# Kernel optimization log

Measured on AMD Instinct MI355X. Metric: run time of the kernel, lower is better.

Reference implementation:

```python
import jax, jax.numpy as jnp
import numpy as np

B, S, E = 4, 2048, 768
DFF = 4 * E
EPS = 1e-5


def _layernorm(x, g, b):
    mu = jnp.mean(x, axis=-1, keepdims=True)
    var = jnp.mean(jnp.square(x - mu), axis=-1, keepdims=True)
    return (x - mu) * jax.lax.rsqrt(var + EPS) * g + b


def setup_inputs() -> dict:
    key = jax.random.key(0)
    ks = jax.random.split(key, 16)
    w = lambda k, shp: jax.random.normal(k, shp, dtype=jnp.float32) * 0.02
    inp = {
        "x": jax.random.normal(ks[0], (B, S, E), dtype=jnp.float32),
        "kv": jax.random.normal(ks[1], (B, S, E), dtype=jnp.float32),
        "wq_w": w(ks[2], (E, E)), "wq_b": jnp.zeros((E,), jnp.float32),
        "wk_w": w(ks[3], (E, E)), "wk_b": jnp.zeros((E,), jnp.float32),
        "wv_w": w(ks[4], (E, E)), "wv_b": jnp.zeros((E,), jnp.float32),
        "ln1_g": jnp.ones((E,), jnp.float32), "ln1_b": jnp.zeros((E,), jnp.float32),
        "wq2_w": w(ks[5], (E, E)), "wq2_b": jnp.zeros((E,), jnp.float32),
        "wk2_w": w(ks[6], (E, E)), "wk2_b": jnp.zeros((E,), jnp.float32),
        "wv2_w": w(ks[7], (E, E)), "wv2_b": jnp.zeros((E,), jnp.float32),
        "ln2_g": jnp.ones((E,), jnp.float32), "ln2_b": jnp.zeros((E,), jnp.float32),
        "w1": w(ks[8], (DFF, E)), "b1": jnp.zeros((DFF,), jnp.float32),
        "w2": w(ks[9], (E, DFF)), "b2": jnp.zeros((E,), jnp.float32),
        "ln3_g": jnp.ones((E,), jnp.float32), "ln3_b": jnp.zeros((E,), jnp.float32),
    }
    return inp


def reference(x, kv, wq_w, wq_b, wk_w, wk_b, wv_w, wv_b, ln1_g, ln1_b,
              wq2_w, wq2_b, wk2_w, wk2_b, wv2_w, wv2_b, ln2_g, ln2_b,
              w1, b1, w2, b2, ln3_g, ln3_b):
    scalar = 1.0 / np.sqrt(E).astype(np.float32)
    mask_value = jnp.finfo(x.dtype).min
    s = x.shape[1]
    causal = jnp.triu(jnp.ones((s, s), dtype=bool), k=1)  # True above diagonal -> masked

    # ---- causal self-attention (single head, full E) ----
    q = x @ wq_w.T + wq_b
    k = x @ wk_w.T + wk_b
    v = x @ wv_w.T + wv_b
    scores = jnp.einsum('bqe,bke->bqk', q, k) * scalar
    scores = jnp.where(causal, mask_value, scores)
    h1 = jnp.einsum('bqk,bke->bqe', jax.nn.softmax(scores, axis=-1), v)
    x = _layernorm(x + h1, ln1_g, ln1_b)

    # ---- cross-attention over kv (no mask) ----
    q2 = x @ wq2_w.T + wq2_b
    k2 = kv @ wk2_w.T + wk2_b
    v2 = kv @ wv2_w.T + wv2_b
    scores2 = jnp.einsum('bqe,bke->bqk', q2, k2) * scalar
    h2 = jnp.einsum('bqk,bke->bqe', jax.nn.softmax(scores2, axis=-1), v2)
    x = _layernorm(x + h2, ln2_g, ln2_b)

    # ---- MLP: Linear -> ReLU -> Linear -> ReLU (note trailing ReLU) ----
    h = jax.nn.relu(x @ w1.T + b1)
    mlp = jax.nn.relu(h @ w2.T + b2)
    return _layernorm(x + mlp, ln3_g, ln3_b)
```

## Files before the change

### kernel.cpp

```cpp
#include <hip/hip_runtime.h>
#include <hip/hip_bf16.h>
#include <math.h>


typedef __bf16 bf16_t;
typedef bf16_t bf16x8 __attribute__((ext_vector_type(8)));
typedef float f32x4 __attribute__((ext_vector_type(4)));

#define TBM 128
#define TBN 128
#define TBK 32
#define CPAD 136

struct MMDesc {
    const bf16_t* A;
    const bf16_t* B;
    const float* bias;
    __hip_bfloat16* C;
    float* lsum;
    int koff;
    int trans;
};
struct MMArgs { MMDesc g[8]; };

__device__ __forceinline__ void load16(const bf16_t* g, bf16_t* l) {
    __builtin_amdgcn_global_load_lds(
        (const __attribute__((address_space(1))) unsigned int*)g,
        (__attribute__((address_space(3))) unsigned int*)l, 16, 0, 0);
}

__device__ __forceinline__ void mm_core(
    const bf16_t* Ag, const bf16_t* Bg, int lda, int ldb, int K,
    bf16_t* Asm, bf16_t* Bsm, int w, int l, int wm, int wn, f32x4 acc[4][4]) {
    const int fr = l & 15;
    const int kq = (l >> 4) * 8;
    const long rsA = (long)64 * lda, rsB = (long)64 * ldb;
    bf16_t* Al = Asm + w * 512;
    bf16_t* Bl = Bsm + w * 512;

    for (int k0 = 0; k0 < K; k0 += 64) {
        load16(Ag + k0, Al);
        load16(Ag + rsA + k0, Al + 2048);
        load16(Bg + k0, Bl);
        load16(Bg + rsB + k0, Bl + 2048);
        load16(Ag + k0 + 32, Al + 4096);
        load16(Ag + rsA + k0 + 32, Al + 6144);
        load16(Bg + k0 + 32, Bl + 4096);
        load16(Bg + rsB + k0 + 32, Bl + 6144);
        __syncthreads();

#pragma unroll
        for (int t = 0; t < 2; ++t) {
            const bf16_t* As = Asm + t * 4096;
            const bf16_t* Bs = Bsm + t * 4096;
            bf16x8 af[4], bfr[4];
#pragma unroll
            for (int i = 0; i < 4; ++i)
                af[i] = *(const bf16x8*)(As + (wm + i * 16 + fr) * TBK + kq);
#pragma unroll
            for (int j = 0; j < 4; ++j)
                bfr[j] = *(const bf16x8*)(Bs + (wn + j * 16 + fr) * TBK + kq);
#pragma unroll
            for (int i = 0; i < 4; ++i)
#pragma unroll
                for (int j = 0; j < 4; ++j)
                    acc[i][j] = __builtin_amdgcn_mfma_f32_16x16x32_bf16(
                        af[i], bfr[j], acc[i][j], 0, 0, 0);
        }
        __syncthreads();
    }
}

__device__ __forceinline__ void tile_out(
    const __hip_bfloat16* ct, __hip_bfloat16* base, long ldc, int tid) {
#pragma unroll
    for (int u = 0; u < 8; ++u) {
        const int e = u * 2048 + tid * 8;
        const int rl = e >> 7, cl = e & 127;
        *(uint4*)(base + (long)rl * ldc + cl) = *(const uint4*)(ct + rl * CPAD + cl);
    }
}

template <bool RELU, bool CLAMPK>
__global__ __launch_bounds__(256) void mm_std(
    MMArgs args, int M, int N, int K, int lda, int ldb, float scale, int GX) {
    __shared__ __align__(16) bf16_t smem[128 * CPAD];
    bf16_t* Asm = smem;
    bf16_t* Bsm = smem + 8192;

    const MMDesc dsc = args.g[blockIdx.z];

    const int lin = blockIdx.x;
    const int panel = lin / (8 * GX);
    const int rem = lin - panel * 8 * GX;
    const int bx = rem >> 3;
    const int by = panel * 8 + (rem & 7);

    const int m0 = by * TBM, n0 = bx * TBN;
    const int tid = threadIdx.x, w = tid >> 6, l = tid & 63;
    const int wm = (w >> 1) * 64, wn = (w & 1) * 64;
    const int srow = w * 16 + (l >> 2);
    const int scol = (l & 3) * 8;
    const int fr = l & 15;

    f32x4 acc[4][4];
    const f32x4 z4 = {0.f, 0.f, 0.f, 0.f};
#pragma unroll
    for (int i = 0; i < 4; ++i)
#pragma unroll
        for (int j = 0; j < 4; ++j) acc[i][j] = z4;

    int Keff = K;
    if (CLAMPK) {
        int km = (by + 1) * TBM - dsc.koff;
        Keff = km < K ? km : K;
    }
    if (!CLAMPK || Keff > 0)
        mm_core(dsc.A + (long)(m0 + srow) * lda + scol,
                dsc.B + (long)(n0 + srow) * ldb + scol,
                lda, ldb, Keff, Asm, Bsm, w, l, wm, wn, acc);

    __hip_bfloat16* ct = (__hip_bfloat16*)smem;
    const int erow = (l >> 4) * 4;
#pragma unroll
    for (int j = 0; j < 4; ++j) {
        const int cl = wn + j * 16 + fr;
        const float bv = dsc.bias ? dsc.bias[n0 + cl] : 0.f;
#pragma unroll
        for (int i = 0; i < 4; ++i) {
            const int rl = wm + i * 16 + erow;
#pragma unroll
            for (int r = 0; r < 4; ++r) {
                float v = acc[i][j][r] * scale + bv;
                if (RELU) v = fmaxf(v, 0.f);
                const int idx = dsc.trans ? (cl * CPAD + rl + r) : ((rl + r) * CPAD + cl);
                ct[idx] = __float2bfloat16(v);
            }
        }
    }
    __syncthreads();
    __hip_bfloat16* base;
    long ldc;
    if (dsc.trans) {
        base = dsc.C + ((long)(m0 >> 11) * N + n0) * 2048 + (m0 & 2047);
        ldc = 2048;
    } else {
        base = dsc.C + (long)m0 * N + n0;
        ldc = N;
    }
    tile_out(ct, base, ldc, tid);
}

template <bool CAUSAL>
__global__ __launch_bounds__(256) void mm_exp(
    MMArgs args, int N, int K, int lda, int ldb, float scale, int GX) {
    __shared__ __align__(16) bf16_t smem[128 * CPAD];
    bf16_t* Asm = smem;
    bf16_t* Bsm = smem + 8192;

    const MMDesc dsc = args.g[blockIdx.z];

    int bx, by;
    if (CAUSAL) {
        const int t = blockIdx.x;
        by = (int)((sqrtf(8.f * t + 1.f) - 1.f) * 0.5f);
        while ((by + 1) * (by + 2) / 2 <= t) ++by;
        while (by * (by + 1) / 2 > t) --by;
        bx = t - by * (by + 1) / 2;
    } else {
        const int lin = blockIdx.x;
        const int panel = lin / (8 * GX);
        const int rem = lin - panel * 8 * GX;
        bx = rem >> 3;
        by = panel * 8 + (rem & 7);
    }

    const int m0 = by * TBM, n0 = bx * TBN;
    const int tid = threadIdx.x, w = tid >> 6, l = tid & 63;
    const int wm = (w >> 1) * 64, wn = (w & 1) * 64;
    const int srow = w * 16 + (l >> 2);
    const int scol = (l & 3) * 8;
    const int fr = l & 15;

    f32x4 acc[4][4];
    const f32x4 z4 = {0.f, 0.f, 0.f, 0.f};
#pragma unroll
    for (int i = 0; i < 4; ++i)
#pragma unroll
        for (int j = 0; j < 4; ++j) acc[i][j] = z4;

    mm_core(dsc.A + (long)(m0 + srow) * lda + scol,
            dsc.B + (long)(n0 + srow) * ldb + scol,
            lda, ldb, K, Asm, Bsm, w, l, wm, wn, acc);

    __hip_bfloat16* ct = (__hip_bfloat16*)smem;
    const int erow = (l >> 4) * 4;
#pragma unroll
    for (int i = 0; i < 4; ++i) {
#pragma unroll
        for (int r = 0; r < 4; ++r) {
            const int rl = wm + i * 16 + erow + r;
            const int grow = m0 + rl;
            float rs = 0.f;
#pragma unroll
            for (int j = 0; j < 4; ++j) {
                const int cl = wn + j * 16 + fr;
                float e;
                if (CAUSAL && (n0 + cl) > grow)
                    e = 0.f;
                else
                    e = __expf(acc[i][j][r] * scale);
                ct[rl * CPAD + cl] = __float2bfloat16(e);
                rs += e;
            }
#pragma unroll
            for (int o = 8; o > 0; o >>= 1) rs += __shfl_down(rs, o, 16);
            if ((l & 15) == 0) atomicAdd(&dsc.lsum[grow], rs);
        }
    }
    __syncthreads();
    tile_out(ct, dsc.C + (long)m0 * N + n0, N, tid);
}

__device__ __forceinline__ float waveReduceSum(float v) {
#pragma unroll
    for (int o = 32; o > 0; o >>= 1) v += __shfl_down(v, o, 64);
    return v;
}
__device__ __forceinline__ float blockReduceSum(float v, float* s) {
    int lane = threadIdx.x & 63, w = threadIdx.x >> 6;
    v = waveReduceSum(v);
    __syncthreads();
    if (lane == 0) s[w] = v;
    __syncthreads();
    return s[0] + s[1] + s[2] + s[3];
}

template <bool BR, bool XF32>
__global__ __launch_bounds__(256) void ln_kernel(
    const float* __restrict__ xf, const __hip_bfloat16* __restrict__ xh,
    const __hip_bfloat16* __restrict__ h1, const __hip_bfloat16* __restrict__ h2,
    const float* __restrict__ hbias, const float* __restrict__ lsum,
    const float* __restrict__ g, const float* __restrict__ beta,
    float* __restrict__ outf, __hip_bfloat16* __restrict__ outb) {
    __shared__ float red[4];
    const int E = 768;
    const long row = blockIdx.x;
    const float hscale = lsum ? (1.f / lsum[row]) : 1.f;

    float vals[3];
    float sum = 0.f;
#pragma unroll
    for (int i = 0; i < 3; ++i) {
        int c = threadIdx.x + i * 256;
        float t = __bfloat162float(h1[row * E + c]) + __bfloat162float(h2[row * E + c]);
        if (BR) t = fmaxf(t + hbias[c], 0.f);
        else t *= hscale;
        float xv = XF32 ? xf[row * E + c] : __bfloat162float(xh[row * E + c]);
        vals[i] = xv + t;
        sum += vals[i];
    }
    sum = blockReduceSum(sum, red);
    const float mean = sum * (1.f / 768.f);

    float ss = 0.f;
#pragma unroll
    for (int i = 0; i < 3; ++i) {
        float d = vals[i] - mean;
        ss += d * d;
    }
    ss = blockReduceSum(ss, red);
    const float inv = rsqrtf(ss * (1.f / 768.f) + 1e-5f);

#pragma unroll
    for (int i = 0; i < 3; ++i) {
        int c = threadIdx.x + i * 256;
        float v = (vals[i] - mean) * inv * g[c] + beta[c];
        if (outf) outf[row * E + c] = v;
        if (outb) outb[row * E + c] = __float2bfloat16(v);
    }
}

struct CvtPtrs {
    const float* s[10];
    __hip_bfloat16* d[10];
};
__global__ __launch_bounds__(256) void cvt_all(CvtPtrs p) {
    int bid = blockIdx.x, seg, off;
    if (bid < 3456) {
        seg = bid / 576;
        off = (bid % 576) * 1024;
    } else if (bid < 8064) {
        int t = bid - 3456;
        seg = 6 + t / 2304;
        off = (t % 2304) * 1024;
    } else {
        int t = bid - 8064;
        seg = 8 + t / 6144;
        off = (t % 6144) * 1024;
    }
    const float* s = p.s[seg];
    __hip_bfloat16* d = p.d[seg];
    int i = off + threadIdx.x * 4;
    float4 v = *(const float4*)(s + i);
    d[i + 0] = __float2bfloat16(v.x);
    d[i + 1] = __float2bfloat16(v.y);
    d[i + 2] = __float2bfloat16(v.z);
    d[i + 3] = __float2bfloat16(v.w);
}

extern "C" void kernel_launch(void* const* d_in, const int* in_sizes, int n_in,
                              void* d_out, int out_size, void* d_ws, size_t ws_size,
                              hipStream_t stream) {
    const int Bb = 4, S = 2048, E = 768, DFF = 3072;
    const int Nr = Bb * S;

    const float* x    = (const float*)d_in[0];
    const float* kv   = (const float*)d_in[1];
    const float* wq_w = (const float*)d_in[2];
    const float* wq_b = (const float*)d_in[3];
    const float* wk_w = (const float*)d_in[4];
    const float* wk_b = (const float*)d_in[5];
    const float* wv_w = (const float*)d_in[6];
    const float* wv_b = (const float*)d_in[7];
    const float* ln1g = (const float*)d_in[8];
    const float* ln1b = (const float*)d_in[9];
    const float* wq2w = (const float*)d_in[10];
    const float* wq2b = (const float*)d_in[11];
    const float* wk2w = (const float*)d_in[12];
    const float* wk2b = (const float*)d_in[13];
    const float* wv2w = (const float*)d_in[14];
    const float* wv2b = (const float*)d_in[15];
    const float* ln2g = (const float*)d_in[16];
    const float* ln2b = (const float*)d_in[17];
    const float* w1   = (const float*)d_in[18];
    const float* b1   = (const float*)d_in[19];
    const float* w2   = (const float*)d_in[20];
    const float* b2   = (const float*)d_in[21];
    const float* ln3g = (const float*)d_in[22];
    const float* ln3b = (const float*)d_in[23];
    float* out = (float*)d_out;

    char* wsp = (char*)d_ws;
    auto alloc = [&](size_t bytes) {
        char* p = wsp;
        wsp += (bytes + 255) & ~(size_t)255;
        return p;
    };
    const size_t nSE = (size_t)Nr * E;
    const size_t nSS = (size_t)Bb * S * S;
    __hip_bfloat16* Pb   = (__hip_bfloat16*)alloc(nSS * 2);
    __hip_bfloat16* qb   = (__hip_bfloat16*)alloc(nSE * 2);
    __hip_bfloat16* kb   = (__hip_bfloat16*)alloc(nSE * 2);
    __hip_bfloat16* hffb = Pb;
    __hip_bfloat16* vtb  = (__hip_bfloat16*)alloc(nSE * 2);
    __hip_bfloat16* xb   = (__hip_bfloat16*)alloc(nSE * 2);
    __hip_bfloat16* kvb  = (__hip_bfloat16*)alloc(nSE * 2);
    __hip_bfloat16* actb = (__hip_bfloat16*)alloc(nSE * 2);
    __hip_bfloat16* hA   = (__hip_bfloat16*)alloc(nSE * 2);
    __hip_bfloat16* hB   = (__hip_bfloat16*)alloc(nSE * 2);
    __hip_bfloat16* wqb   = (__hip_bfloat16*)alloc((size_t)E * E * 2);
    __hip_bfloat16* wkb   = (__hip_bfloat16*)alloc((size_t)E * E * 2);
    __hip_bfloat16* wvb   = (__hip_bfloat16*)alloc((size_t)E * E * 2);
    __hip_bfloat16* wq2bm = (__hip_bfloat16*)alloc((size_t)E * E * 2);
    __hip_bfloat16* wk2bm = (__hip_bfloat16*)alloc((size_t)E * E * 2);
    __hip_bfloat16* wv2bm = (__hip_bfloat16*)alloc((size_t)E * E * 2);
    __hip_bfloat16* w1b   = (__hip_bfloat16*)alloc((size_t)DFF * E * 2);
    __hip_bfloat16* w2b   = (__hip_bfloat16*)alloc((size_t)E * DFF * 2);
    float* lsum1 = (float*)alloc((size_t)Nr * 4);
    float* lsum2 = (float*)alloc((size_t)Nr * 4);

    const float scale = 1.0f / sqrtf((float)E);
    const dim3 blk(256);

    hipMemsetAsync(lsum1, 0, (size_t)Nr * 4 * 2, stream);

    CvtPtrs cp;
    cp.s[0] = wq_w; cp.d[0] = wqb;
    cp.s[1] = wk_w; cp.d[1] = wkb;
    cp.s[2] = wv_w; cp.d[2] = wvb;
    cp.s[3] = wq2w; cp.d[3] = wq2bm;
    cp.s[4] = wk2w; cp.d[4] = wk2bm;
    cp.s[5] = wv2w; cp.d[5] = wv2bm;
    cp.s[6] = w1;   cp.d[6] = w1b;
    cp.s[7] = w2;   cp.d[7] = w2b;
    cp.s[8] = x;    cp.d[8] = xb;
    cp.s[9] = kv;   cp.d[9] = kvb;
    cvt_all<<<8064 + 12288, blk, 0, stream>>>(cp);

    {
        MMArgs a{};
        a.g[0] = {(const bf16_t*)xb, (const bf16_t*)wqb, wq_b, qb, nullptr, 0, 0};
        a.g[1] = {(const bf16_t*)xb, (const bf16_t*)wkb, wk_b, kb, nullptr, 0, 0};
        a.g[2] = {(const bf16_t*)xb, (const bf16_t*)wvb, wv_b, vtb, nullptr, 0, 1};
        mm_std<false, false><<<dim3(6 * 64, 1, 3), blk, 0, stream>>>(
            a, Nr, E, E, E, E, 1.f, 6);
    }
    {
        MMArgs a{};
        for (int b = 0; b < 4; ++b)
            a.g[b] = {(const bf16_t*)qb + (long)b * S * E,
                      (const bf16_t*)kb + (long)b * S * E, nullptr,
                      Pb + (long)b * S * S, lsum1 + b * S, 0, 0};
        mm_exp<true><<<dim3(136, 1, 4), blk, 0, stream>>>(a, S, E, E, E, scale, 16);
    }
    {
        MMArgs a{};
        for (int b = 0; b < 4; ++b)
            for (int ks = 0; ks < 2; ++ks)
                a.g[b * 2 + ks] = {(const bf16_t*)Pb + (long)b * S * S + ks * 1024,
                                   (const bf16_t*)vtb + (long)b * E * S + ks * 1024,
                                   nullptr, (ks ? hB : hA) + (long)b * S * E,
                                   nullptr, ks * 1024, 0};
        mm_std<false, true><<<dim3(6 * 16, 1, 8), blk, 0, stream>>>(
            a, S, E, 1024, S, S, 1.f, 6);
    }
    ln_kernel<false, true><<<Nr, blk, 0, stream>>>(
        x, nullptr, hA, hB, nullptr, lsum1, ln1g, ln1b, nullptr, actb);

    {
        MMArgs a{};
        a.g[0] = {(const bf16_t*)actb, (const bf16_t*)wq2bm, wq2b, qb, nullptr, 0, 0};
        a.g[1] = {(const bf16_t*)kvb, (const bf16_t*)wk2bm, wk2b, kb, nullptr, 0, 0};
        a.g[2] = {(const bf16_t*)kvb, (const bf16_t*)wv2bm, wv2b, vtb, nullptr, 0, 1};
        mm_std<false, false><<<dim3(6 * 64, 1, 3), blk, 0, stream>>>(
            a, Nr, E, E, E, E, 1.f, 6);
    }
    {
        MMArgs a{};
        for (int b = 0; b < 4; ++b)
            a.g[b] = {(const bf16_t*)qb + (long)b * S * E,
                      (const bf16_t*)kb + (long)b * S * E, nullptr,
                      Pb + (long)b * S * S, lsum2 + b * S, 0, 0};
        mm_exp<false><<<dim3(16 * 16, 1, 4), blk, 0, stream>>>(a, S, E, E, E, scale, 16);
    }
    {
        MMArgs a{};
        for (int b = 0; b < 4; ++b)
            for (int ks = 0; ks < 2; ++ks)
                a.g[b * 2 + ks] = {(const bf16_t*)Pb + (long)b * S * S + ks * 1024,
                                   (const bf16_t*)vtb + (long)b * E * S + ks * 1024,
                                   nullptr, (ks ? hB : hA) + (long)b * S * E,
                                   nullptr, 0, 0};
        mm_std<false, false><<<dim3(6 * 16, 1, 8), blk, 0, stream>>>(
            a, S, E, 1024, S, S, 1.f, 6);
    }
    ln_kernel<false, false><<<Nr, blk, 0, stream>>>(
        nullptr, actb, hA, hB, nullptr, lsum2, ln2g, ln2b, nullptr, actb);

    {
        MMArgs a{};
        a.g[0] = {(const bf16_t*)actb, (const bf16_t*)w1b, b1, hffb, nullptr, 0, 0};
        mm_std<true, false><<<dim3(24 * 64, 1, 1), blk, 0, stream>>>(
            a, Nr, DFF, E, E, E, 1.f, 24);
    }
    {
        MMArgs a{};
        a.g[0] = {(const bf16_t*)hffb, (const bf16_t*)w2b, nullptr, hA, nullptr, 0, 0};
        a.g[1] = {(const bf16_t*)hffb + 1536, (const bf16_t*)w2b + 1536, nullptr,
                  hB, nullptr, 0, 0};
        mm_std<false, false><<<dim3(6 * 64, 1, 2), blk, 0, stream>>>(
            a, Nr, E, 1536, DFF, DFF, 1.f, 6);
    }
    ln_kernel<true, false><<<Nr, blk, 0, stream>>>(
        nullptr, actb, hA, hB, b2, nullptr, ln3g, ln3b, out, nullptr);
}
```

Before: 548.5 us.

## Store GEMM operands in pre-tiled 128x32 blocked layout for contiguous LDS loads

All bf16 operand buffers (weights, activations, Q/K/V^T, P) are now written in a blocked layout of 128-row by 32-column tiles with k-groups of 8 laid out contiguously. Each global_load_lds then reads a fully contiguous 4KB chunk instead of strided rows. The conversion kernel, the GEMM epilogues and the layernorm writers are rewritten to emit this layout. The aim is better global memory coalescing and simpler addressing, at the cost of more complex index math in the producers and a layout coupling that every stage has to honour.

```diff
diff --git a/kernel.cpp b/kernel.cpp
--- a/kernel.cpp
+++ b/kernel.cpp
@@ -9,7 +9,6 @@
 
 #define TBM 128
 #define TBN 128
-#define TBK 32
 #define CPAD 136
 
 struct MMDesc {
@@ -19,7 +18,7 @@
     __hip_bfloat16* C;
     float* lsum;
     int koff;
-    int trans;
+    int mode;
 };
 struct MMArgs { MMDesc g[8]; };
 
@@ -30,23 +29,24 @@
 }
 
 __device__ __forceinline__ void mm_core(
-    const bf16_t* Ag, const bf16_t* Bg, int lda, int ldb, int K,
+    const bf16_t* At, const bf16_t* Bt, int K,
     bf16_t* Asm, bf16_t* Bsm, int w, int l, int wm, int wn, f32x4 acc[4][4]) {
+    const int go = w * 1024 + l * 8;
+    const int lo = w * 1024;
     const int fr = l & 15;
-    const int kq = (l >> 4) * 8;
-    const long rsA = (long)64 * lda, rsB = (long)64 * ldb;
-    bf16_t* Al = Asm + w * 512;
-    bf16_t* Bl = Bsm + w * 512;
+    const int kg = (l >> 4) * 1024;
 
     for (int k0 = 0; k0 < K; k0 += 64) {
-        load16(Ag + k0, Al);
-        load16(Ag + rsA + k0, Al + 2048);
-        load16(Bg + k0, Bl);
-        load16(Bg + rsB + k0, Bl + 2048);
-        load16(Ag + k0 + 32, Al + 4096);
-        load16(Ag + rsA + k0 + 32, Al + 6144);
-        load16(Bg + k0 + 32, Bl + 4096);
-        load16(Bg + rsB + k0 + 32, Bl + 6144);
+        const bf16_t* a = At + (long)(k0 >> 5) * 4096;
+        const bf16_t* b = Bt + (long)(k0 >> 5) * 4096;
+        load16(a + go, Asm + lo);
+        load16(a + go + 512, Asm + lo + 512);
+        load16(b + go, Bsm + lo);
+        load16(b + go + 512, Bsm + lo + 512);
+        load16(a + go + 4096, Asm + lo + 4096);
+        load16(a + go + 4608, Asm + lo + 4608);
+        load16(b + go + 4096, Bsm + lo + 4096);
+        load16(b + go + 4608, Bsm + lo + 4608);
         __syncthreads();
 
 #pragma unroll
@@ -56,10 +56,10 @@
             bf16x8 af[4], bfr[4];
 #pragma unroll
             for (int i = 0; i < 4; ++i)
-                af[i] = *(const bf16x8*)(As + (wm + i * 16 + fr) * TBK + kq);
+                af[i] = *(const bf16x8*)(As + kg + (wm + i * 16 + fr) * 8);
 #pragma unroll
             for (int j = 0; j < 4; ++j)
-                bfr[j] = *(const bf16x8*)(Bs + (wn + j * 16 + fr) * TBK + kq);
+                bfr[j] = *(const bf16x8*)(Bs + kg + (wn + j * 16 + fr) * 8);
 #pragma unroll
             for (int i = 0; i < 4; ++i)
 #pragma unroll
@@ -71,19 +71,28 @@
     }
 }
 
-__device__ __forceinline__ void tile_out(
-    const __hip_bfloat16* ct, __hip_bfloat16* base, long ldc, int tid) {
+__device__ __forceinline__ void tile_out_row(
+    const __hip_bfloat16* ct, __hip_bfloat16* base, int N, int tid) {
 #pragma unroll
     for (int u = 0; u < 8; ++u) {
         const int e = u * 2048 + tid * 8;
         const int rl = e >> 7, cl = e & 127;
-        *(uint4*)(base + (long)rl * ldc + cl) = *(const uint4*)(ct + rl * CPAD + cl);
+        *(uint4*)(base + (long)rl * N + cl) = *(const uint4*)(ct + rl * CPAD + cl);
+    }
+}
+__device__ __forceinline__ void tile_out_tiled(
+    const __hip_bfloat16* ct, __hip_bfloat16* tb, int tid) {
+#pragma unroll
+    for (int u = 0; u < 8; ++u) {
+        const int idx = u * 256 + tid;
+        const int r = idx & 127, sk = idx >> 7;
+        *(uint4*)(tb + (long)sk * 1024 + r * 8) = *(const uint4*)(ct + r * CPAD + sk * 8);
     }
 }
 
 template <bool RELU, bool CLAMPK>
 __global__ __launch_bounds__(256) void mm_std(
-    MMArgs args, int M, int N, int K, int lda, int ldb, float scale, int GX) {
+    MMArgs args, int N, int K, int ldtA, int ldtB, float scale, int GX) {
     __shared__ __align__(16) bf16_t smem[128 * CPAD];
     bf16_t* Asm = smem;
     bf16_t* Bsm = smem + 8192;
@@ -99,8 +108,6 @@
     const int m0 = by * TBM, n0 = bx * TBN;
     const int tid = threadIdx.x, w = tid >> 6, l = tid & 63;
     const int wm = (w >> 1) * 64, wn = (w & 1) * 64;
-    const int srow = w * 16 + (l >> 2);
-    const int scol = (l & 3) * 8;
     const int fr = l & 15;
 
     f32x4 acc[4][4];
@@ -116,9 +123,9 @@
         Keff = km < K ? km : K;
     }
     if (!CLAMPK || Keff > 0)
-        mm_core(dsc.A + (long)(m0 + srow) * lda + scol,
-                dsc.B + (long)(n0 + srow) * ldb + scol,
-                lda, ldb, Keff, Asm, Bsm, w, l, wm, wn, acc);
+        mm_core(dsc.A + (long)(m0 >> 7) * ldtA * 4096,
+                dsc.B + (long)(n0 >> 7) * ldtB * 4096,
+                Keff, Asm, Bsm, w, l, wm, wn, acc);
 
     __hip_bfloat16* ct = (__hip_bfloat16*)smem;
     const int erow = (l >> 4) * 4;
@@ -133,27 +140,27 @@
             for (int r = 0; r < 4; ++r) {
                 float v = acc[i][j][r] * scale + bv;
                 if (RELU) v = fmaxf(v, 0.f);
-                const int idx = dsc.trans ? (cl * CPAD + rl + r) : ((rl + r) * CPAD + cl);
+                const int idx = (dsc.mode == 2) ? (cl * CPAD + rl + r)
+                                                : ((rl + r) * CPAD + cl);
                 ct[idx] = __float2bfloat16(v);
             }
         }
     }
     __syncthreads();
-    __hip_bfloat16* base;
-    long ldc;
-    if (dsc.trans) {
-        base = dsc.C + ((long)(m0 >> 11) * N + n0) * 2048 + (m0 & 2047);
-        ldc = 2048;
+    if (dsc.mode == 0) {
+        tile_out_row(ct, dsc.C + (long)m0 * N + n0, N, tid);
+    } else if (dsc.mode == 1) {
+        tile_out_tiled(ct, dsc.C + ((long)(m0 >> 7) * (N >> 5) + (n0 >> 5)) * 4096, tid);
     } else {
-        base = dsc.C + (long)m0 * N + n0;
-        ldc = N;
-    }
-    tile_out(ct, base, ldc, tid);
+        __hip_bfloat16* tb = dsc.C + (long)(m0 >> 11) * N * 2048 +
+                             ((long)(n0 >> 7) * 64 + ((m0 & 2047) >> 5)) * 4096;
+        tile_out_tiled(ct, tb, tid);
+    }
 }
 
 template <bool CAUSAL>
 __global__ __launch_bounds__(256) void mm_exp(
-    MMArgs args, int N, int K, int lda, int ldb, float scale, int GX) {
+    MMArgs args, int N, int K, int ldtA, int ldtB, float scale, int GX) {
     __shared__ __align__(16) bf16_t smem[128 * CPAD];
     bf16_t* Asm = smem;
     bf16_t* Bsm = smem + 8192;
@@ -178,8 +185,6 @@
     const int m0 = by * TBM, n0 = bx * TBN;
     const int tid = threadIdx.x, w = tid >> 6, l = tid & 63;
     const int wm = (w >> 1) * 64, wn = (w & 1) * 64;
-    const int srow = w * 16 + (l >> 2);
-    const int scol = (l & 3) * 8;
     const int fr = l & 15;
 
     f32x4 acc[4][4];
@@ -189,9 +194,9 @@
 #pragma unroll
         for (int j = 0; j < 4; ++j) acc[i][j] = z4;
 
-    mm_core(dsc.A + (long)(m0 + srow) * lda + scol,
-            dsc.B + (long)(n0 + srow) * ldb + scol,
-            lda, ldb, K, Asm, Bsm, w, l, wm, wn, acc);
+    mm_core(dsc.A + (long)(m0 >> 7) * ldtA * 4096,
+            dsc.B + (long)(n0 >> 7) * ldtB * 4096,
+            K, Asm, Bsm, w, l, wm, wn, acc);
 
     __hip_bfloat16* ct = (__hip_bfloat16*)smem;
     const int erow = (l >> 4) * 4;
@@ -219,7 +224,7 @@
         }
     }
     __syncthreads();
-    tile_out(ct, dsc.C + (long)m0 * N + n0, N, tid);
+    tile_out_tiled(ct, dsc.C + ((long)(m0 >> 7) * (N >> 5) + (n0 >> 5)) * 4096, tid);
 }
 
 __device__ __forceinline__ float waveReduceSum(float v) {
@@ -234,6 +239,11 @@
     if (lane == 0) s[w] = v;
     __syncthreads();
     return s[0] + s[1] + s[2] + s[3];
+}
+
+__device__ __forceinline__ long tidx768(long row, int c) {
+    return ((row >> 7) * 24 + (c >> 5)) * 4096 + ((c & 31) >> 3) * 1024 +
+           (row & 127) * 8 + (c & 7);
 }
 
 template <bool BR, bool XF32>
@@ -256,7 +266,7 @@
         float t = __bfloat162float(h1[row * E + c]) + __bfloat162float(h2[row * E + c]);
         if (BR) t = fmaxf(t + hbias[c], 0.f);
         else t *= hscale;
-        float xv = XF32 ? xf[row * E + c] : __bfloat162float(xh[row * E + c]);
+        float xv = XF32 ? xf[row * E + c] : __bfloat162float(xh[tidx768(row, c)]);
         vals[i] = xv + t;
         sum += vals[i];
     }
@@ -277,36 +287,45 @@
         int c = threadIdx.x + i * 256;
         float v = (vals[i] - mean) * inv * g[c] + beta[c];
         if (outf) outf[row * E + c] = v;
-        if (outb) outb[row * E + c] = __float2bfloat16(v);
-    }
-}
-
-struct CvtPtrs {
+        if (outb) outb[tidx768(row, c)] = __float2bfloat16(v);
+    }
+}
+
+struct CvtArgs {
     const float* s[10];
     __hip_bfloat16* d[10];
+    int cols[10];
+    int start[11];
 };
-__global__ __launch_bounds__(256) void cvt_all(CvtPtrs p) {
-    int bid = blockIdx.x, seg, off;
-    if (bid < 3456) {
-        seg = bid / 576;
-        off = (bid % 576) * 1024;
-    } else if (bid < 8064) {
-        int t = bid - 3456;
-        seg = 6 + t / 2304;
-        off = (t % 2304) * 1024;
-    } else {
-        int t = bid - 8064;
-        seg = 8 + t / 6144;
-        off = (t % 6144) * 1024;
-    }
-    const float* s = p.s[seg];
-    __hip_bfloat16* d = p.d[seg];
-    int i = off + threadIdx.x * 4;
-    float4 v = *(const float4*)(s + i);
-    d[i + 0] = __float2bfloat16(v.x);
-    d[i + 1] = __float2bfloat16(v.y);
-    d[i + 2] = __float2bfloat16(v.z);
-    d[i + 3] = __float2bfloat16(v.w);
+__global__ __launch_bounds__(256) void cvt_all(CvtArgs a) {
+    const int t = blockIdx.x;
+    int i = 0;
+    while (t >= a.start[i + 1]) ++i;
+    const int local = t - a.start[i];
+    const int C = a.cols[i];
+    const int tpr = C >> 5;
+    const int tr = local / tpr, tc = local - tr * tpr;
+    const float* src = a.s[i] + (long)tr * 128 * C + tc * 32;
+    __hip_bfloat16* dst = a.d[i] + (long)local * 4096;
+
+#pragma unroll
+    for (int it = 0; it < 2; ++it) {
+        const int u = threadIdx.x + it * 256;
+        const int r = u >> 2, kgp = u & 3;
+        const float* sp = src + (long)r * C + kgp * 8;
+        float4 v0 = *(const float4*)sp;
+        float4 v1 = *(const float4*)(sp + 4);
+        union { __hip_bfloat16 h[8]; uint4 q; } tmp;
+        tmp.h[0] = __float2bfloat16(v0.x);
+        tmp.h[1] = __float2bfloat16(v0.y);
+        tmp.h[2] = __float2bfloat16(v0.z);
+        tmp.h[3] = __float2bfloat16(v0.w);
+        tmp.h[4] = __float2bfloat16(v1.x);
+        tmp.h[5] = __float2bfloat16(v1.y);
+        tmp.h[6] = __float2bfloat16(v1.z);
+        tmp.h[7] = __float2bfloat16(v1.w);
+        *(uint4*)(dst + kgp * 1024 + r * 8) = tmp.q;
+    }
 }
 
 extern "C" void kernel_launch(void* const* d_in, const int* in_sizes, int n_in,
@@ -375,92 +394,95 @@
 
     hipMemsetAsync(lsum1, 0, (size_t)Nr * 4 * 2, stream);
 
-    CvtPtrs cp;
-    cp.s[0] = wq_w; cp.d[0] = wqb;
-    cp.s[1] = wk_w; cp.d[1] = wkb;
-    cp.s[2] = wv_w; cp.d[2] = wvb;
-    cp.s[3] = wq2w; cp.d[3] = wq2bm;
-    cp.s[4] = wk2w; cp.d[4] = wk2bm;
-    cp.s[5] = wv2w; cp.d[5] = wv2bm;
-    cp.s[6] = w1;   cp.d[6] = w1b;
-    cp.s[7] = w2;   cp.d[7] = w2b;
-    cp.s[8] = x;    cp.d[8] = xb;
-    cp.s[9] = kv;   cp.d[9] = kvb;
-    cvt_all<<<8064 + 12288, blk, 0, stream>>>(cp);
-
-    {
-        MMArgs a{};
-        a.g[0] = {(const bf16_t*)xb, (const bf16_t*)wqb, wq_b, qb, nullptr, 0, 0};
-        a.g[1] = {(const bf16_t*)xb, (const bf16_t*)wkb, wk_b, kb, nullptr, 0, 0};
-        a.g[2] = {(const bf16_t*)xb, (const bf16_t*)wvb, wv_b, vtb, nullptr, 0, 1};
+    CvtArgs ca;
+    const float* srcs[10] = {wq_w, wk_w, wv_w, wq2w, wk2w, wv2w, w1, w2, x, kv};
+    __hip_bfloat16* dsts[10] = {wqb, wkb, wvb, wq2bm, wk2bm, wv2bm, w1b, w2b, xb, kvb};
+    int colv[10] = {768, 768, 768, 768, 768, 768, 768, 3072, 768, 768};
+    int tiles[10] = {144, 144, 144, 144, 144, 144, 576, 576, 1536, 1536};
+    int acc0 = 0;
+    for (int i = 0; i < 10; ++i) {
+        ca.s[i] = srcs[i];
+        ca.d[i] = dsts[i];
+        ca.cols[i] = colv[i];
+        ca.start[i] = acc0;
+        acc0 += tiles[i];
+    }
+    ca.start[10] = acc0;
+    cvt_all<<<acc0, blk, 0, stream>>>(ca);
+
+    {
+        MMArgs a{};
+        a.g[0] = {(const bf16_t*)xb, (const bf16_t*)wqb, wq_b, qb, nullptr, 0, 1};
+        a.g[1] = {(const bf16_t*)xb, (const bf16_t*)wkb, wk_b, kb, nullptr, 0, 1};
+        a.g[2] = {(const bf16_t*)xb, (const bf16_t*)wvb, wv_b, vtb, nullptr, 0, 2};
         mm_std<false, false><<<dim3(6 * 64, 1, 3), blk, 0, stream>>>(
-            a, Nr, E, E, E, E, 1.f, 6);
+            a, E, E, 24, 24, 1.f, 6);
     }
     {
         MMArgs a{};
         for (int b = 0; b < 4; ++b)
             a.g[b] = {(const bf16_t*)qb + (long)b * S * E,
                       (const bf16_t*)kb + (long)b * S * E, nullptr,
-                      Pb + (long)b * S * S, lsum1 + b * S, 0, 0};
-        mm_exp<true><<<dim3(136, 1, 4), blk, 0, stream>>>(a, S, E, E, E, scale, 16);
+                      Pb + (long)b * S * S, lsum1 + b * S, 0, 1};
+        mm_exp<true><<<dim3(136, 1, 4), blk, 0, stream>>>(a, S, E, 24, 24, scale, 16);
     }
     {
         MMArgs a{};
         for (int b = 0; b < 4; ++b)
             for (int ks = 0; ks < 2; ++ks)
-                a.g[b * 2 + ks] = {(const bf16_t*)Pb + (long)b * S * S + ks * 1024,
-                                   (const bf16_t*)vtb + (long)b * E * S + ks * 1024,
+                a.g[b * 2 + ks] = {(const bf16_t*)Pb + (long)b * S * S + ks * 32 * 4096,
+                                   (const bf16_t*)vtb + (long)b * S * E + ks * 32 * 4096,
                                    nullptr, (ks ? hB : hA) + (long)b * S * E,
                                    nullptr, ks * 1024, 0};
         mm_std<false, true><<<dim3(6 * 16, 1, 8), blk, 0, stream>>>(
-            a, S, E, 1024, S, S, 1.f, 6);
+            a, E, 1024, 64, 64, 1.f, 6);
     }
     ln_kernel<false, true><<<Nr, blk, 0, stream>>>(
         x, nullptr, hA, hB, nullptr, lsum1, ln1g, ln1b, nullptr, actb);
 
     {
         MMArgs a{};
-        a.g[0] = {(const bf16_t*)actb, (const bf16_t*)wq2bm, wq2b, qb, nullptr, 0, 0};
-        a.g[1] = {(const bf16_t*)kvb, (const bf16_t*)wk2bm, wk2b, kb, nullptr, 0, 0};
-        a.g[2] = {(const bf16_t*)kvb, (const bf16_t*)wv2bm, wv2b, vtb, nullptr, 0, 1};
+        a.g[0] = {(const bf16_t*)actb, (const bf16_t*)wq2bm, wq2b, qb, nullptr, 0, 1};
+        a.g[1] = {(const bf16_t*)kvb, (const bf16_t*)wk2bm, wk2b, kb, nullptr, 0, 1};
+        a.g[2] = {(const bf16_t*)kvb, (const bf16_t*)wv2bm, wv2b, vtb, nullptr, 0, 2};
         mm_std<false, false><<<dim3(6 * 64, 1, 3), blk, 0, stream>>>(
-            a, Nr, E, E, E, E, 1.f, 6);
+            a, E, E, 24, 24, 1.f, 6);
     }
     {
         MMArgs a{};
         for (int b = 0; b < 4; ++b)
             a.g[b] = {(const bf16_t*)qb + (long)b * S * E,
                       (const bf16_t*)kb + (long)b * S * E, nullptr,
-                      Pb + (long)b * S * S, lsum2 + b * S, 0, 0};
-        mm_exp<false><<<dim3(16 * 16, 1, 4), blk, 0, stream>>>(a, S, E, E, E, scale, 16);
+                      Pb + (long)b * S * S, lsum2 + b * S, 0, 1};
+        mm_exp<false><<<dim3(16 * 16, 1, 4), blk, 0, stream>>>(a, S, E, 24, 24, scale, 16);
     }
     {
         MMArgs a{};
         for (int b = 0; b < 4; ++b)
             for (int ks = 0; ks < 2; ++ks)
-                a.g[b * 2 + ks] = {(const bf16_t*)Pb + (long)b * S * S + ks * 1024,
-                                   (const bf16_t*)vtb + (long)b * E * S + ks * 1024,
+                a.g[b * 2 + ks] = {(const bf16_t*)Pb + (long)b * S * S + ks * 32 * 4096,
+                                   (const bf16_t*)vtb + (long)b * S * E + ks * 32 * 4096,
                                    nullptr, (ks ? hB : hA) + (long)b * S * E,
                                    nullptr, 0, 0};
         mm_std<false, false><<<dim3(6 * 16, 1, 8), blk, 0, stream>>>(
-            a, S, E, 1024, S, S, 1.f, 6);
+            a, E, 1024, 64, 64, 1.f, 6);
     }
     ln_kernel<false, false><<<Nr, blk, 0, stream>>>(
         nullptr, actb, hA, hB, nullptr, lsum2, ln2g, ln2b, nullptr, actb);
 
     {
         MMArgs a{};
-        a.g[0] = {(const bf16_t*)actb, (const bf16_t*)w1b, b1, hffb, nullptr, 0, 0};
+        a.g[0] = {(const bf16_t*)actb, (const bf16_t*)w1b, b1, hffb, nullptr, 0, 1};
         mm_std<true, false><<<dim3(24 * 64, 1, 1), blk, 0, stream>>>(
-            a, Nr, DFF, E, E, E, 1.f, 24);
+            a, DFF, E, 24, 24, 1.f, 24);
     }
     {
         MMArgs a{};
         a.g[0] = {(const bf16_t*)hffb, (const bf16_t*)w2b, nullptr, hA, nullptr, 0, 0};
-        a.g[1] = {(const bf16_t*)hffb + 1536, (const bf16_t*)w2b + 1536, nullptr,
-                  hB, nullptr, 0, 0};
+        a.g[1] = {(const bf16_t*)hffb + 48 * 4096, (const bf16_t*)w2b + 48 * 4096,
+                  nullptr, hB, nullptr, 0, 0};
         mm_std<false, false><<<dim3(6 * 64, 1, 2), blk, 0, stream>>>(
-            a, Nr, E, 1536, DFF, DFF, 1.f, 6);
+            a, E, 1536, 96, 96, 1.f, 6);
     }
     ln_kernel<true, false><<<Nr, blk, 0, stream>>>(
         nullptr, actb, hA, hB, b2, nullptr, ln3g, ln3b, out, nullptr);
```

New measurement: 568.7 us. 1.04x slower.
